# Optimization experiments

Measured on AMD Instinct MI355X. Metric: run time of the kernel, lower is better.

The kernel has to match this reference:

```python
import jax, jax.numpy as jnp
import numpy as np

D_MODEL, N_EXPERTS, N_VIEWS, N_TOKENS = 256, 16, 3, 8192

def setup_inputs() -> dict:
    key = jax.random.key(0)
    ks = jax.random.split(key, 10)
    s = 0.05
    return {
        "v0": jax.random.normal(ks[0], (N_TOKENS, D_MODEL), jnp.float32),
        "v1": jax.random.normal(ks[1], (N_TOKENS, D_MODEL), jnp.float32),
        "v2": jax.random.normal(ks[2], (N_TOKENS, D_MODEL), jnp.float32),
        "router_w": jax.random.normal(ks[3], (N_VIEWS, N_EXPERTS, D_MODEL), jnp.float32) * s,
        "expert_keys": jax.random.normal(ks[4], (N_EXPERTS, D_MODEL), jnp.float32) * s,
        "W1": jax.random.normal(ks[5], (N_EXPERTS, D_MODEL, 4 * D_MODEL), jnp.float32) * s,
        "b1": jax.random.normal(ks[6], (N_EXPERTS, 4 * D_MODEL), jnp.float32) * s,
        "W2": jax.random.normal(ks[7], (N_EXPERTS, 4 * D_MODEL, D_MODEL), jnp.float32) * s,
        "b2": jax.random.normal(ks[8], (N_EXPERTS, D_MODEL), jnp.float32) * s,
        "top_k": 4,
    }

def _laplace_gate(v, rw, expert_keys, top_k):
    # -||v - key||^2 expanded: -(|v|^2 + |k|^2 - 2 v.k)   -> [N, E]
    sq = (jnp.sum(v * v, -1, keepdims=True)
          + jnp.sum(expert_keys * expert_keys, -1)[None, :]
          - 2.0 * (v @ expert_keys.T))
    logits = -sq + v @ rw.T                      # router(h), no bias
    topv, topi = jax.lax.top_k(logits, top_k)    # [N, K]
    gate = jax.nn.softmax(topv, axis=-1)         # exp(topv - logsumexp(topv))
    return gate, topi

def reference(v0, v1, v2, router_w, expert_keys, W1, b1, W2, b2, top_k):
    views = [v0, v1, v2]
    E = expert_keys.shape[0]
    N = v0.shape[0]
    fused = jnp.zeros_like(v0)
    rows = jnp.arange(N)[:, None]
    for i, v in enumerate(views):
        gate, idx = _laplace_gate(v, router_w[i], expert_keys, top_k)
        # scatter top-k gates into a dense [N, E] combine matrix
        dense_gate = jnp.zeros((N, E), v.dtype).at[rows, idx].add(gate)
        out = jnp.zeros_like(v)
        for e in range(E):  # fixed small expert loop; each token combined via its gate
            h = jax.nn.gelu(v @ W1[e] + b1[e], approximate=False)
            out = out + dense_gate[:, e:e + 1] * (h @ W2[e] + b2[e])
        fused = fused + out
    return fused
```

## Files before the change

kernel.cpp:

```cpp
#include <hip/hip_runtime.h>
#include <math.h>

#define D_MODEL 256
#define N_EXP   16
#define N_VIEWS 3
#define N_TOK   8192
#define TOPK    4
#define HDIM    1024
#define CH      64
#define NCH     16
#define NSUB    32
#define ROWS    64
#define TI_MAX  40
#define NGROUP  48
#define GCAP    8192
#define REC_ELTS 32768

typedef short s16x8 __attribute__((ext_vector_type(8)));
typedef float f32x4 __attribute__((ext_vector_type(4)));

__device__ __forceinline__ unsigned short f2bf(float x) {
    union { float f; unsigned u; } a; a.f = x;
    unsigned r = a.u + 0x7FFFu + ((a.u >> 16) & 1u);
    return (unsigned short)(r >> 16);
}

__device__ __forceinline__ void dma16(const unsigned short* gp, unsigned short* lp) {
    __builtin_amdgcn_global_load_lds(
        (const __attribute__((address_space(1))) unsigned int*)gp,
        (__attribute__((address_space(3))) unsigned int*)lp, 16, 0, 0);
}

__device__ __forceinline__ void dma_sub(const unsigned short* wrec0, int sc,
                                        unsigned short* ldst, int wave, int lane) {
    const unsigned short* g = wrec0 + (size_t)(sc >> 1) * REC_ELTS
                                    + (size_t)((wave * 4 + (sc & 1) * 2) * 512);
    dma16(g + lane * 8,       ldst + wave * 1024);
    dma16(g + 512 + lane * 8, ldst + wave * 1024 + 512);
}

#define T1_STRIDE 65
#define T2_STRIDE 257

__global__ __launch_bounds__(256) void prep_kernel(
    const float* __restrict__ v0, const float* __restrict__ v1, const float* __restrict__ v2,
    const float* __restrict__ rw, const float* __restrict__ keys,
    const float* __restrict__ W1, const float* __restrict__ W2,
    unsigned short* __restrict__ Wf, unsigned short* __restrict__ Xbf,
    int* __restrict__ counts, int* __restrict__ rowTok, float* __restrict__ rowGate)
{
    __shared__ __align__(16) char smem[66560];

    int bid = blockIdx.x;
    int tid = threadIdx.x;
    int sept = bid / 7, r7 = bid % 7;

    if (r7 < 4) {
        int wb = sept * 4 + r7;
        int c = wb & 15, e = (wb >> 4) & 15, z = wb >> 8;
        unsigned short* dst = Wf + (size_t)(e * NCH + c) * REC_ELTS;
        if (z == 0) {
            float* T1 = (float*)smem;
            const float* src = W1 + (size_t)e * 256 * 1024 + c * 64;
            #pragma unroll
            for (int p = 0; p < 16; p++) {
                int k = p * 16 + (tid >> 4), c4 = (tid & 15) * 4;
                float4 v = *(const float4*)(src + (size_t)k * 1024 + c4);
                T1[k * T1_STRIDE + c4]     = v.x;
                T1[k * T1_STRIDE + c4 + 1] = v.y;
                T1[k * T1_STRIDE + c4 + 2] = v.z;
                T1[k * T1_STRIDE + c4 + 3] = v.w;
            }
            __syncthreads();
            #pragma unroll
            for (int i = 0; i < 8; i++) {
                int idx = tid + i * 256;
                int lane = idx & 63, nt = (idx >> 6) & 3, ks = idx >> 8;
                int nl = nt * 16 + (lane & 15);
                int kbase = ks * 32 + (lane >> 4) * 8;
                s16x8 o;
                #pragma unroll
                for (int j = 0; j < 8; j++) o[j] = (short)f2bf(T1[(kbase + j) * T1_STRIDE + nl]);
                *(s16x8*)(dst + (size_t)idx * 8) = o;
            }
        } else {
            float* T2 = (float*)smem;
            const float* src = W2 + ((size_t)e * 1024 + c * 64) * 256;
            #pragma unroll
            for (int p = 0; p < 16; p++) {
                int k2l = p * 4 + (tid >> 6), c4 = (tid & 63) * 4;
                float4 v = *(const float4*)(src + (size_t)k2l * 256 + c4);
                T2[k2l * T2_STRIDE + c4]     = v.x;
                T2[k2l * T2_STRIDE + c4 + 1] = v.y;
                T2[k2l * T2_STRIDE + c4 + 2] = v.z;
                T2[k2l * T2_STRIDE + c4 + 3] = v.w;
            }
            __syncthreads();
            dst += 16384;
            #pragma unroll
            for (int i = 0; i < 8; i++) {
                int idx = tid + i * 256;
                int lane = idx & 63, ntile = (idx >> 6) & 15, ks2 = idx >> 10;
                int n = ntile * 16 + (lane & 15);
                int kbase = ks2 * 32 + (lane >> 4) * 8;
                s16x8 o;
                #pragma unroll
                for (int j = 0; j < 8; j++) o[j] = (short)f2bf(T2[(kbase + j) * T2_STRIDE + n]);
                *(s16x8*)(dst + (size_t)idx * 8) = o;
            }
        }
        return;
    }

    int rb = sept * 3 + (r7 - 4);
    float* XsT    = (float*)smem;
    float* cwS    = (float*)(smem + 32768);
    float* logitS = (float*)(smem + 49152);
    float* knS    = (float*)(smem + 53504);
    int*   lcnt   = (int*)(smem + 53568);
    int*   lbase  = (int*)(smem + 53632);
    int*   fpos   = (int*)(smem + 53696);
    int*   eIdx   = (int*)(smem + 53760);
    float* gV     = (float*)(smem + 54784);

    int view = rb >> 7, xb = rb & 127;
    const float* src = view == 0 ? v0 : (view == 1 ? v1 : v2);

    for (int i = tid; i < N_EXP * D_MODEL; i += 256)
        cwS[i] = rw[view * N_EXP * D_MODEL + i] + 2.0f * keys[i];
    if (tid < N_EXP) {
        const float4* kp = (const float4*)(keys + tid * D_MODEL);
        float s = 0.f;
        for (int d = 0; d < 64; d++) { float4 k = kp[d]; s += k.x*k.x + k.y*k.y + k.z*k.z + k.w*k.w; }
        knS[tid] = s; lcnt[tid] = 0; fpos[tid] = 0;
    }

    int wave = tid >> 6, lane = tid & 63;
    float a0 = 0.f, a1 = 0.f, a2 = 0.f, a3 = 0.f;

    #pragma unroll 1
    for (int p = 0; p < 2; p++) {
        {
            int t = tid >> 2, q = tid & 3;
            int token = xb * 64 + t;
            const float4* vp = (const float4*)(src + (size_t)token * D_MODEL + p * 128 + q * 32);
            ushort4* xo = (ushort4*)(Xbf + ((size_t)view * N_TOK + token) * D_MODEL + p * 128 + q * 32);
            #pragma unroll
            for (int i = 0; i < 8; i++) {
                float4 v = vp[i];
                ushort4 h; h.x = f2bf(v.x); h.y = f2bf(v.y); h.z = f2bf(v.z); h.w = f2bf(v.w);
                xo[i] = h;
                int d = q * 32 + i * 4;
                XsT[(d + 0) * 64 + t] = v.x;
                XsT[(d + 1) * 64 + t] = v.y;
                XsT[(d + 2) * 64 + t] = v.z;
                XsT[(d + 3) * 64 + t] = v.w;
            }
        }
        __syncthreads();
        {
            const float* xcol = &XsT[lane];
            const float* c0 = &cwS[(wave * 4 + 0) * D_MODEL + p * 128];
            const float* c1 = &cwS[(wave * 4 + 1) * D_MODEL + p * 128];
            const float* c2 = &cwS[(wave * 4 + 2) * D_MODEL + p * 128];
            const float* c3 = &cwS[(wave * 4 + 3) * D_MODEL + p * 128];
            #pragma unroll 4
            for (int d4 = 0; d4 < 32; d4++) {
                float x0 = xcol[(d4 * 4 + 0) * 64];
                float x1 = xcol[(d4 * 4 + 1) * 64];
                float x2 = xcol[(d4 * 4 + 2) * 64];
                float x3 = xcol[(d4 * 4 + 3) * 64];
                float4 w0 = *(const float4*)(c0 + d4 * 4);
                float4 w1 = *(const float4*)(c1 + d4 * 4);
                float4 w2 = *(const float4*)(c2 + d4 * 4);
                float4 w3 = *(const float4*)(c3 + d4 * 4);
                a0 += x0 * w0.x + x1 * w0.y + x2 * w0.z + x3 * w0.w;
                a1 += x0 * w1.x + x1 * w1.y + x2 * w1.z + x3 * w1.w;
                a2 += x0 * w2.x + x1 * w2.y + x2 * w2.z + x3 * w2.w;
                a3 += x0 * w3.x + x1 * w3.y + x2 * w3.z + x3 * w3.w;
            }
        }
        __syncthreads();
    }
    logitS[lane * 17 + wave * 4 + 0] = a0 - knS[wave * 4 + 0];
    logitS[lane * 17 + wave * 4 + 1] = a1 - knS[wave * 4 + 1];
    logitS[lane * 17 + wave * 4 + 2] = a2 - knS[wave * 4 + 2];
    logitS[lane * 17 + wave * 4 + 3] = a3 - knS[wave * 4 + 3];
    __syncthreads();

    if (tid < 64) {
        int tl = tid;
        float lg[N_EXP];
        #pragma unroll
        for (int e = 0; e < N_EXP; e++) lg[e] = logitS[tl * 17 + e];
        int idxs[TOPK]; float vals[TOPK];
        #pragma unroll
        for (int k = 0; k < TOPK; k++) {
            float best = -1e30f; int bi = 0;
            #pragma unroll
            for (int e = 0; e < N_EXP; e++)
                if (lg[e] > best) { best = lg[e]; bi = e; }
            idxs[k] = bi; vals[k] = best;
            #pragma unroll
            for (int e = 0; e < N_EXP; e++)
                lg[e] = (e == bi) ? -1e30f : lg[e];
        }
        float m = vals[0], s = 0.f, ex[TOPK];
        #pragma unroll
        for (int k = 0; k < TOPK; k++) { ex[k] = __expf(vals[k] - m); s += ex[k]; }
        float inv = 1.0f / s;
        #pragma unroll
        for (int k = 0; k < TOPK; k++) {
            eIdx[tl * 4 + k] = idxs[k];
            gV[tl * 4 + k]   = ex[k] * inv;
            atomicAdd(&lcnt[idxs[k]], 1);
        }
    }
    __syncthreads();
    if (tid < N_EXP)
        lbase[tid] = lcnt[tid] ? atomicAdd(&counts[view * N_EXP + tid], lcnt[tid]) : 0;
    __syncthreads();
    {
        int e  = eIdx[tid];
        float gv = gV[tid];
        int pos = atomicAdd(&fpos[e], 1);
        int dst = (view * N_EXP + e) * GCAP + lbase[e] + pos;
        rowTok[dst]  = xb * 64 + (tid >> 2);
        rowGate[dst] = gv;
    }
}

__global__ __launch_bounds__(512, 4) void ffn_kernel(
    const unsigned short* __restrict__ Xbf, const unsigned short* __restrict__ Wf,
    const float* __restrict__ b1, const float* __restrict__ b2,
    const int* __restrict__ counts, const int* __restrict__ rowTok,
    const float* __restrict__ rowGate, float* __restrict__ out)
{
    __shared__ __align__(16) unsigned short W1buf[4][8192];
    __shared__ __align__(16) unsigned short Hc[2][2048];

    int s = blockIdx.x;
    int xcd = s & 7, k = s >> 3;
    int j = k % 6, ti = k / 6;
    int e = 2 * xcd + (j & 1), view = j >> 1;
    int g = view * N_EXP + e;
    int L = counts[g];
    int r0 = ti * ROWS;
    if (r0 >= L) return;
    int base = g * GCAP;

    int tid = threadIdx.x;
    int wave = tid >> 6, lane = tid & 63, lmod = lane & 15, quad = lane >> 4;

    const unsigned short* wchunk = Wf + (size_t)e * NCH * REC_ELTS;

    int mt1 = wave & 3, nh = wave >> 2;
    int ms  = wave & 1, ns = wave >> 1;

    s16x8 areg[8];
    {
        int gr = r0 + mt1 * 16 + lmod;
        int token = (gr < L) ? rowTok[base + gr] : 0;
        const unsigned short* xp = Xbf + ((size_t)view * N_TOK + token) * D_MODEL;
        #pragma unroll
        for (int ks = 0; ks < 8; ks++)
            areg[ks] = *(const s16x8*)(xp + ks * 32 + quad * 8);
    }
    float bbCur = b1[e * HDIM + nh * 16 + lmod];

    f32x4 acc2[2][4];
    #pragma unroll
    for (int i = 0; i < 2; i++)
        #pragma unroll
        for (int jj = 0; jj < 4; jj++) acc2[i][jj] = (f32x4){0.f, 0.f, 0.f, 0.f};

    __builtin_amdgcn_sched_barrier(0);
    dma_sub(wchunk, 0, &W1buf[0][0], wave, lane);
    __builtin_amdgcn_sched_barrier(0);
    dma_sub(wchunk, 1, &W1buf[1][0], wave, lane);
    __builtin_amdgcn_sched_barrier(0);
    dma_sub(wchunk, 2, &W1buf[2][0], wave, lane);
    __builtin_amdgcn_sched_barrier(0);
    asm volatile("s_waitcnt vmcnt(4)" ::: "memory");
    __builtin_amdgcn_sched_barrier(0);
    __builtin_amdgcn_s_barrier();
    __builtin_amdgcn_sched_barrier(0);

    s16x8 w2r[4] = {};

    #pragma unroll 1
    for (int cc = 0; cc < NSUB; cc++) {
        int bn = (cc + 1 < NSUB) ? cc + 1 : NSUB - 1;
        float bbNext = b1[e * HDIM + bn * 32 + nh * 16 + lmod];

        const unsigned short* w1s = &W1buf[cc & 3][0];
        f32x4 a1a = (f32x4){0.f, 0.f, 0.f, 0.f};
        f32x4 a1b = (f32x4){0.f, 0.f, 0.f, 0.f};
        __builtin_amdgcn_s_setprio(1);
        #pragma unroll
        for (int ks = 0; ks < 8; ks += 2) {
            s16x8 bw0 = *(const s16x8*)(w1s + ks * 1024 + nh * 512 + lane * 8);
            s16x8 bw1 = *(const s16x8*)(w1s + (ks + 1) * 1024 + nh * 512 + lane * 8);
            a1a = __builtin_amdgcn_mfma_f32_16x16x32_bf16(areg[ks],     bw0, a1a, 0, 0, 0);
            a1b = __builtin_amdgcn_mfma_f32_16x16x32_bf16(areg[ks + 1], bw1, a1b, 0, 0, 0);
        }
        __builtin_amdgcn_s_setprio(0);

        {
            unsigned short* hd = &Hc[cc & 1][0];
            int bo = mt1 * 512 + (nh * 2 + (lmod >> 3)) * 128 + quad * 32 + (lmod & 7);
            #pragma unroll
            for (int r = 0; r < 4; r++) {
                float h = a1a[r] + a1b[r] + bbCur;
                float u = h * (0.7978845608f + 0.0356774081f * h * h);
                float ex2 = __expf(2.f * u);
                float tn = 1.f - 2.f * __builtin_amdgcn_rcpf(1.f + ex2);
                hd[bo + r * 8] = f2bf(0.5f * h * (1.f + tn));
            }
        }

        if (cc > 0) {
            const unsigned short* hs = &Hc[(cc - 1) & 1][0];
            s16x8 afr[2];
            #pragma unroll
            for (int mt = 0; mt < 2; mt++)
                afr[mt] = *(const s16x8*)(hs + ((ms * 2 + mt) * 64 + lane) * 8);
            __builtin_amdgcn_s_setprio(1);
            #pragma unroll
            for (int nt = 0; nt < 4; nt++)
                #pragma unroll
                for (int mt = 0; mt < 2; mt++)
                    acc2[mt][nt] = __builtin_amdgcn_mfma_f32_16x16x32_bf16(
                        afr[mt], w2r[nt], acc2[mt][nt], 0, 0, 0);
            __builtin_amdgcn_s_setprio(0);
        }

        {
            const unsigned short* w2p = wchunk + (size_t)(cc >> 1) * REC_ELTS + 16384
                                        + (size_t)(((cc & 1) * 16 + ns * 4) * 512);
            #pragma unroll
            for (int nt = 0; nt < 4; nt++)
                w2r[nt] = *(const s16x8*)(w2p + nt * 512 + lane * 8);
        }

        __builtin_amdgcn_sched_barrier(0);
        if (cc + 3 < NSUB)
            dma_sub(wchunk, cc + 3, &W1buf[(cc + 3) & 3][0], wave, lane);
        __builtin_amdgcn_sched_barrier(0);

        bbCur = bbNext;

        asm volatile("s_waitcnt vmcnt(9) lgkmcnt(0)" ::: "memory");
        __builtin_amdgcn_sched_barrier(0);
        __builtin_amdgcn_s_barrier();
        __builtin_amdgcn_sched_barrier(0);
    }

    asm volatile("s_waitcnt vmcnt(0)" ::: "memory");

    {
        const unsigned short* hs = &Hc[(NSUB - 1) & 1][0];
        s16x8 afr[2];
        #pragma unroll
        for (int mt = 0; mt < 2; mt++)
            afr[mt] = *(const s16x8*)(hs + ((ms * 2 + mt) * 64 + lane) * 8);
        #pragma unroll
        for (int nt = 0; nt < 4; nt++)
            #pragma unroll
            for (int mt = 0; mt < 2; mt++)
                acc2[mt][nt] = __builtin_amdgcn_mfma_f32_16x16x32_bf16(
                    afr[mt], w2r[nt], acc2[mt][nt], 0, 0, 0);
    }

    int   tokR[2][4];
    float gateR[2][4];
    #pragma unroll
    for (int mt = 0; mt < 2; mt++)
        #pragma unroll
        for (int r = 0; r < 4; r++) {
            int gr = r0 + (ms * 2 + mt) * 16 + quad * 4 + r;
            bool ok = gr < L;
            tokR[mt][r]  = ok ? rowTok[base + gr] : -1;
            gateR[mt][r] = ok ? rowGate[base + gr] : 0.f;
        }
    #pragma unroll
    for (int nt = 0; nt < 4; nt++) {
        int col = (ns * 4 + nt) * 16 + lmod;
        float b2v = b2[e * D_MODEL + col];
        #pragma unroll
        for (int mt = 0; mt < 2; mt++) {
            #pragma unroll
            for (int r = 0; r < 4; r++) {
                if (tokR[mt][r] >= 0) {
                    atomicAdd(&out[(size_t)tokR[mt][r] * D_MODEL + col],
                              gateR[mt][r] * (acc2[mt][nt][r] + b2v));
                }
            }
        }
    }
}

extern "C" void kernel_launch(void* const* d_in, const int* in_sizes, int n_in,
                              void* d_out, int out_size, void* d_ws, size_t ws_size,
                              hipStream_t stream)
{
    const float* v0   = (const float*)d_in[0];
    const float* v1   = (const float*)d_in[1];
    const float* v2   = (const float*)d_in[2];
    const float* rw   = (const float*)d_in[3];
    const float* keys = (const float*)d_in[4];
    const float* W1   = (const float*)d_in[5];
    const float* b1   = (const float*)d_in[6];
    const float* W2   = (const float*)d_in[7];
    const float* b2   = (const float*)d_in[8];
    float* out = (float*)d_out;

    char* p = (char*)d_ws;
    unsigned short* Xbf = (unsigned short*)p; p += (size_t)N_VIEWS * N_TOK * D_MODEL * 2;
    unsigned short* Wf  = (unsigned short*)p; p += (size_t)N_EXP * NCH * REC_ELTS * 2;
    int*   counts = (int*)p;   p += 256;
    int*   rowTok = (int*)p;   p += (size_t)NGROUP * GCAP * 4;
    float* rowGate= (float*)p; p += (size_t)NGROUP * GCAP * 4;

    hipMemsetAsync(counts, 0, NGROUP * sizeof(int), stream);
    hipMemsetAsync(out, 0, (size_t)out_size * sizeof(float), stream);

    prep_kernel<<<896, 256, 0, stream>>>(v0, v1, v2, rw, keys, W1, W2,
                                         Wf, Xbf, counts, rowTok, rowGate);
    ffn_kernel<<<8 * 6 * TI_MAX, 512, 0, stream>>>(Xbf, Wf, b1, b2, counts,
                                                   rowTok, rowGate, out);
}
```

Before: 320.9 us.

## Double FFN row tile to 128 tokens per block to halve weight traffic

Each FFN block now processes 128 gathered token rows instead of 64. Every wave computes two 16-row M tiles against the same W1 fragment and eight W2 N-tiles, so each weight load is reused across twice as many rows. This halves the number of blocks per expert and with it the repeated W1/W2 streaming from global memory. In exchange, register pressure rises (launch bounds drop to 2 blocks per CU), there are fewer blocks to spread across CUs, and the Hc shared buffer doubles.

```diff
diff --git a/kernel.cpp b/kernel.cpp
--- a/kernel.cpp
+++ b/kernel.cpp
@@ -10,8 +10,8 @@
 #define CH      64
 #define NCH     16
 #define NSUB    32
-#define ROWS    64
-#define TI_MAX  40
+#define ROWS    128
+#define TI_MAX  20
 #define NGROUP  48
 #define GCAP    8192
 #define REC_ELTS 32768
@@ -230,14 +230,14 @@
     }
 }
 
-__global__ __launch_bounds__(512, 4) void ffn_kernel(
+__global__ __launch_bounds__(512, 2) void ffn_kernel(
     const unsigned short* __restrict__ Xbf, const unsigned short* __restrict__ Wf,
     const float* __restrict__ b1, const float* __restrict__ b2,
     const int* __restrict__ counts, const int* __restrict__ rowTok,
     const float* __restrict__ rowGate, float* __restrict__ out)
 {
     __shared__ __align__(16) unsigned short W1buf[4][8192];
-    __shared__ __align__(16) unsigned short Hc[2][2048];
+    __shared__ __align__(16) unsigned short Hc[2][4096];
 
     int s = blockIdx.x;
     int xcd = s & 7, k = s >> 3;
@@ -254,25 +254,25 @@
 
     const unsigned short* wchunk = Wf + (size_t)e * NCH * REC_ELTS;
 
-    int mt1 = wave & 3, nh = wave >> 2;
-    int ms  = wave & 1, ns = wave >> 1;
-
-    s16x8 areg[8];
-    {
-        int gr = r0 + mt1 * 16 + lmod;
+    int mt = wave & 3, nh = wave >> 2;
+
+    s16x8 areg[2][8];
+    #pragma unroll
+    for (int m = 0; m < 2; m++) {
+        int gr = r0 + mt * 32 + m * 16 + lmod;
         int token = (gr < L) ? rowTok[base + gr] : 0;
         const unsigned short* xp = Xbf + ((size_t)view * N_TOK + token) * D_MODEL;
         #pragma unroll
         for (int ks = 0; ks < 8; ks++)
-            areg[ks] = *(const s16x8*)(xp + ks * 32 + quad * 8);
+            areg[m][ks] = *(const s16x8*)(xp + ks * 32 + quad * 8);
     }
     float bbCur = b1[e * HDIM + nh * 16 + lmod];
 
-    f32x4 acc2[2][4];
+    f32x4 acc2[2][8];
     #pragma unroll
-    for (int i = 0; i < 2; i++)
-        #pragma unroll
-        for (int jj = 0; jj < 4; jj++) acc2[i][jj] = (f32x4){0.f, 0.f, 0.f, 0.f};
+    for (int m = 0; m < 2; m++)
+        #pragma unroll
+        for (int nt = 0; nt < 8; nt++) acc2[m][nt] = (f32x4){0.f, 0.f, 0.f, 0.f};
 
     __builtin_amdgcn_sched_barrier(0);
     dma_sub(wchunk, 0, &W1buf[0][0], wave, lane);
@@ -286,7 +286,7 @@
     __builtin_amdgcn_s_barrier();
     __builtin_amdgcn_sched_barrier(0);
 
-    s16x8 w2r[4] = {};
+    s16x8 w2r[8] = {};
 
     #pragma unroll 1
     for (int cc = 0; cc < NSUB; cc++) {
@@ -294,28 +294,31 @@
         float bbNext = b1[e * HDIM + bn * 32 + nh * 16 + lmod];
 
         const unsigned short* w1s = &W1buf[cc & 3][0];
-        f32x4 a1a = (f32x4){0.f, 0.f, 0.f, 0.f};
-        f32x4 a1b = (f32x4){0.f, 0.f, 0.f, 0.f};
+        f32x4 a1[2];
+        a1[0] = (f32x4){0.f, 0.f, 0.f, 0.f};
+        a1[1] = (f32x4){0.f, 0.f, 0.f, 0.f};
         __builtin_amdgcn_s_setprio(1);
         #pragma unroll
-        for (int ks = 0; ks < 8; ks += 2) {
-            s16x8 bw0 = *(const s16x8*)(w1s + ks * 1024 + nh * 512 + lane * 8);
-            s16x8 bw1 = *(const s16x8*)(w1s + (ks + 1) * 1024 + nh * 512 + lane * 8);
-            a1a = __builtin_amdgcn_mfma_f32_16x16x32_bf16(areg[ks],     bw0, a1a, 0, 0, 0);
-            a1b = __builtin_amdgcn_mfma_f32_16x16x32_bf16(areg[ks + 1], bw1, a1b, 0, 0, 0);
+        for (int ks = 0; ks < 8; ks++) {
+            s16x8 bw = *(const s16x8*)(w1s + ks * 1024 + nh * 512 + lane * 8);
+            a1[0] = __builtin_amdgcn_mfma_f32_16x16x32_bf16(areg[0][ks], bw, a1[0], 0, 0, 0);
+            a1[1] = __builtin_amdgcn_mfma_f32_16x16x32_bf16(areg[1][ks], bw, a1[1], 0, 0, 0);
         }
         __builtin_amdgcn_s_setprio(0);
 
         {
             unsigned short* hd = &Hc[cc & 1][0];
-            int bo = mt1 * 512 + (nh * 2 + (lmod >> 3)) * 128 + quad * 32 + (lmod & 7);
-            #pragma unroll
-            for (int r = 0; r < 4; r++) {
-                float h = a1a[r] + a1b[r] + bbCur;
-                float u = h * (0.7978845608f + 0.0356774081f * h * h);
-                float ex2 = __expf(2.f * u);
-                float tn = 1.f - 2.f * __builtin_amdgcn_rcpf(1.f + ex2);
-                hd[bo + r * 8] = f2bf(0.5f * h * (1.f + tn));
+            #pragma unroll
+            for (int m = 0; m < 2; m++) {
+                int bo = (mt * 2 + m) * 512 + (nh * 2 + (lmod >> 3)) * 128 + quad * 32 + (lmod & 7);
+                #pragma unroll
+                for (int r = 0; r < 4; r++) {
+                    float h = a1[m][r] + bbCur;
+                    float u = h * (0.7978845608f + 0.0356774081f * h * h);
+                    float ex2 = __expf(2.f * u);
+                    float tn = 1.f - 2.f * __builtin_amdgcn_rcpf(1.f + ex2);
+                    hd[bo + r * 8] = f2bf(0.5f * h * (1.f + tn));
+                }
             }
         }
 
@@ -323,24 +326,24 @@
             const unsigned short* hs = &Hc[(cc - 1) & 1][0];
             s16x8 afr[2];
             #pragma unroll
-            for (int mt = 0; mt < 2; mt++)
-                afr[mt] = *(const s16x8*)(hs + ((ms * 2 + mt) * 64 + lane) * 8);
+            for (int m = 0; m < 2; m++)
+                afr[m] = *(const s16x8*)(hs + ((mt * 2 + m) * 64 + lane) * 8);
             __builtin_amdgcn_s_setprio(1);
             #pragma unroll
-            for (int nt = 0; nt < 4; nt++)
+            for (int nt = 0; nt < 8; nt++)
                 #pragma unroll
-                for (int mt = 0; mt < 2; mt++)
-                    acc2[mt][nt] = __builtin_amdgcn_mfma_f32_16x16x32_bf16(
-                        afr[mt], w2r[nt], acc2[mt][nt], 0, 0, 0);
+                for (int m = 0; m < 2; m++)
+                    acc2[m][nt] = __builtin_amdgcn_mfma_f32_16x16x32_bf16(
+                        afr[m], w2r[nt], acc2[m][nt], 0, 0, 0);
             __builtin_amdgcn_s_setprio(0);
         }
 
         {
-            const unsigned short* w2p = wchunk + (size_t)(cc >> 1) * REC_ELTS + 16384
-                                        + (size_t)(((cc & 1) * 16 + ns * 4) * 512);
-            #pragma unroll
-            for (int nt = 0; nt < 4; nt++)
-                w2r[nt] = *(const s16x8*)(w2p + nt * 512 + lane * 8);
+            const unsigned short* w2p = wchunk + (size_t)(cc >> 1) * REC_ELTS + 16384;
+            #pragma unroll
+            for (int nt = 0; nt < 8; nt++)
+                w2r[nt] = *(const s16x8*)(w2p
+                    + (size_t)((((cc & 1) * 16 + nh * 8 + nt) * 64 + lane)) * 8);
         }
 
         __builtin_amdgcn_sched_barrier(0);
@@ -350,7 +353,7 @@
 
         bbCur = bbNext;
 
-        asm volatile("s_waitcnt vmcnt(9) lgkmcnt(0)" ::: "memory");
+        asm volatile("s_waitcnt vmcnt(13) lgkmcnt(0)" ::: "memory");
         __builtin_amdgcn_sched_barrier(0);
         __builtin_amdgcn_s_barrier();
         __builtin_amdgcn_sched_barrier(0);
@@ -362,38 +365,38 @@
         const unsigned short* hs = &Hc[(NSUB - 1) & 1][0];
         s16x8 afr[2];
         #pragma unroll
-        for (int mt = 0; mt < 2; mt++)
-            afr[mt] = *(const s16x8*)(hs + ((ms * 2 + mt) * 64 + lane) * 8);
-        #pragma unroll
-        for (int nt = 0; nt < 4; nt++)
-            #pragma unroll
-            for (int mt = 0; mt < 2; mt++)
-                acc2[mt][nt] = __builtin_amdgcn_mfma_f32_16x16x32_bf16(
-                    afr[mt], w2r[nt], acc2[mt][nt], 0, 0, 0);
+        for (int m = 0; m < 2; m++)
+            afr[m] = *(const s16x8*)(hs + ((mt * 2 + m) * 64 + lane) * 8);
+        #pragma unroll
+        for (int nt = 0; nt < 8; nt++)
+            #pragma unroll
+            for (int m = 0; m < 2; m++)
+                acc2[m][nt] = __builtin_amdgcn_mfma_f32_16x16x32_bf16(
+                    afr[m], w2r[nt], acc2[m][nt], 0, 0, 0);
     }
 
     int   tokR[2][4];
     float gateR[2][4];
     #pragma unroll
-    for (int mt = 0; mt < 2; mt++)
+    for (int m = 0; m < 2; m++)
         #pragma unroll
         for (int r = 0; r < 4; r++) {
-            int gr = r0 + (ms * 2 + mt) * 16 + quad * 4 + r;
+            int gr = r0 + mt * 32 + m * 16 + quad * 4 + r;
             bool ok = gr < L;
-            tokR[mt][r]  = ok ? rowTok[base + gr] : -1;
-            gateR[mt][r] = ok ? rowGate[base + gr] : 0.f;
+            tokR[m][r]  = ok ? rowTok[base + gr] : -1;
+            gateR[m][r] = ok ? rowGate[base + gr] : 0.f;
         }
     #pragma unroll
-    for (int nt = 0; nt < 4; nt++) {
-        int col = (ns * 4 + nt) * 16 + lmod;
+    for (int nt = 0; nt < 8; nt++) {
+        int col = nh * 128 + nt * 16 + lmod;
         float b2v = b2[e * D_MODEL + col];
         #pragma unroll
-        for (int mt = 0; mt < 2; mt++) {
+        for (int m = 0; m < 2; m++) {
             #pragma unroll
             for (int r = 0; r < 4; r++) {
-                if (tokR[mt][r] >= 0) {
-                    atomicAdd(&out[(size_t)tokR[mt][r] * D_MODEL + col],
-                              gateR[mt][r] * (acc2[mt][nt][r] + b2v));
+                if (tokR[m][r] >= 0) {
+                    atomicAdd(&out[(size_t)tokR[m][r] * D_MODEL + col],
+                              gateR[m][r] * (acc2[m][nt][r] + b2v));
                 }
             }
         }
```

After: 407.8 us. 27.1% more time.
